# Kernel tuning notes

Hardware: AMD Instinct MI355X
Metric: run time of the kernel (lower is better)

## Reference

```python
import jax, jax.numpy as jnp
import numpy as np

N = 50000   # num_node
E = 1600000 # edge_size (N * avg_degree 32)
B = 64      # batch, hardcoded via repeat(64,1,1) in the torch module


def setup_inputs() -> dict:
    key = jax.random.key(0)
    k = jax.random.split(key, 8)
    return {
        "t": jax.random.normal(k[0], (1,), dtype=jnp.float32),
        "input": jax.random.normal(k[1], (B, N), dtype=jnp.float32),
        "edge_i": jax.random.randint(k[2], (E,), 0, N, dtype=jnp.int32),
        "edge_j": jax.random.randint(k[3], (E,), 0, N, dtype=jnp.int32),
        "weight_react": jax.random.normal(k[4], (1, E), dtype=jnp.float32) / 10.0,
        "weight_diff": jax.random.normal(k[5], (1, E), dtype=jnp.float32) / 1000.0,
        "bias_reaction": jax.random.normal(k[6], (1, N), dtype=jnp.float32) / 10.0,
        "bias_diffusion": jax.random.normal(k[7], (1, N), dtype=jnp.float32) / 10.0,
    }


def _lap_matvec(x, w, src, dst, n):
    # W[src_e, dst_e] = w_e (duplicates coalesce by sum, as torch sparse_coo_tensor does)
    # L = diag(colsum(W)) - W ; returns x @ L^T applied batched: out[b, v] = (L x[b])[v]
    col = jax.ops.segment_sum(w, dst, num_segments=n)                 # [N] column sums
    msg = jax.ops.segment_sum(w[:, None] * x[:, dst].T, src,
                              num_segments=n)                          # [N, B]
    return col[None, :] * x - msg.T                                   # [B, N]


def reference(t, input, edge_i, edge_j, weight_react, weight_diff,
              bias_reaction, bias_diffusion):
    x = input                                                          # [B, N]
    n = x.shape[1]
    # reaction Laplacian uses edges (i -> j); diffusion uses transposed (j -> i)
    reaction = _lap_matvec(x, weight_react[0], edge_i, edge_j, n) + bias_reaction
    diffusion = _lap_matvec(x, weight_diff[0], edge_j, edge_i, n) + bias_diffusion
    # up and down both True: tanh(reaction) + diffusion + input
    return jnp.tanh(reaction) + diffusion + x
```

## Files before the change

kernel.cpp:

```cpp
#include <hip/hip_runtime.h>
#include <hip/hip_fp16.h>


#define BKT_SHIFT 7
#define BKT_NODES 128
#define RCAP 4608
#define CH 4096
#define NBP 512

#define RFL(x) __builtin_amdgcn_readfirstlane(x)

__device__ __forceinline__ unsigned bf16_rne(float f) {
    unsigned u = __float_as_uint(f);
    unsigned rb = (u >> 16) & 1u;
    u += 0x7FFFu + rb;
    return u >> 16;
}
__device__ __forceinline__ float bf16_lo(int y) {
    return __uint_as_float(((unsigned)y) << 16);
}

__global__ void zero_kernel(float4* __restrict__ p, int n4) {
    int i = blockIdx.x * blockDim.x + threadIdx.x;
    int s = gridDim.x * blockDim.x;
    float4 z = make_float4(0.f, 0.f, 0.f, 0.f);
    for (; i < n4; i += s) p[i] = z;
}

__global__ void transpose_kernel(const float* __restrict__ x, float* __restrict__ xt,
                                 __half* __restrict__ xth, int N) {
    __shared__ float tile[64][65];
    int v0 = blockIdx.x * 64;
    int tx = threadIdx.x;
    int ty = threadIdx.y;
    if (v0 + tx < N) {
        for (int b = ty; b < 64; b += 16)
            tile[tx][b] = x[b * N + v0 + tx];
    }
    __syncthreads();
    for (int vl = ty; vl < 64; vl += 16) {
        int v = v0 + vl;
        if (v < N) {
            float val = tile[vl][tx];
            xt[(size_t)v * 64 + tx] = val;
            xth[(size_t)v * 64 + tx] = __float2half(val);
        }
    }
}

__global__ void __launch_bounds__(512) partition_kernel(
        const int* __restrict__ ei, const int* __restrict__ ej,
        const float* __restrict__ wr, const float* __restrict__ wd,
        int* __restrict__ gcur, int2* __restrict__ runs,
        int E, int NB) {
    __shared__ int cnt[2 * NBP];
    __shared__ int base_a[2 * NBP];
    __shared__ int gb[2 * NBP];
    __shared__ int2 buf[2 * CH];

    int tid = threadIdx.x;
    int e0 = blockIdx.x * CH;
    int ch_len = min(CH, E - e0);
    if (ch_len <= 0) return;

    for (int b = tid; b < 2 * NBP; b += 512) cnt[b] = 0;
    __syncthreads();
    for (int t = tid; t < ch_len; t += 512) {
        int i = ei[e0 + t], j = ej[e0 + t];
        atomicAdd(&cnt[i >> BKT_SHIFT], 1);
        atomicAdd(&cnt[NBP + (j >> BKT_SHIFT)], 1);
    }
    __syncthreads();
    if (tid < 64) {
        int carry = 0;
        #pragma unroll
        for (int c = 0; c < (2 * NBP) / 64; ++c) {
            int idx = c * 64 + tid;
            int val = cnt[idx];
            int scan = val;
            for (int off = 1; off < 64; off <<= 1) {
                int n = __shfl_up(scan, off, 64);
                if (tid >= off) scan += n;
            }
            int excl = scan - val + carry;
            base_a[idx] = excl;
            cnt[idx] = excl;
            carry += __shfl(scan, 63, 64);
        }
    }
    __syncthreads();
    for (int t = tid; t < ch_len; t += 512) {
        int e = e0 + t;
        int i = ei[e], j = ej[e];
        float wrv = wr[e], wdv = wd[e];
        unsigned br16 = bf16_rne(wrv), bd16 = bf16_rne(wdv);
        int b0 = i >> BKT_SHIFT;
        int p0 = atomicAdd(&cnt[b0], 1);
        buf[p0] = make_int2((int)(((unsigned)b0 << 23) | ((unsigned)(i & 127) << 16) | (unsigned)j),
                            (int)((br16 << 16) | bd16));
        int b1 = j >> BKT_SHIFT;
        int p1 = atomicAdd(&cnt[NBP + b1], 1);
        buf[p1] = make_int2((int)(((unsigned)b1 << 23) | ((unsigned)(j & 127) << 16) | (unsigned)i),
                            (int)((bd16 << 16) | br16));
    }
    __syncthreads();
    for (int cb = tid; cb < 2 * NBP; cb += 512) {
        int n = cnt[cb] - base_a[cb];
        if (n > 0) {
            int side = cb >> 9;
            int bkt = cb & (NBP - 1);
            gb[cb] = atomicAdd(&gcur[side * NB + bkt], n);
        }
    }
    __syncthreads();
    int total = 2 * ch_len;
    for (int t = tid; t < total; t += 512) {
        int2 p = buf[t];
        int side = (t >= ch_len) ? 1 : 0;
        int bkt = ((unsigned)p.x >> 23) & 0x1FF;
        int cb = side * NBP + bkt;
        int rank = gb[cb] + (t - base_a[cb]);
        if (rank < RCAP)
            runs[((size_t)(side * NB + bkt)) * RCAP + rank] = p;
    }
}

__global__ void __launch_bounds__(512) csr_kernel(
        const int* __restrict__ gcur, int2* __restrict__ runs,
        int4* __restrict__ meta, int NB, int N) {
    __shared__ int cnt[BKT_NODES];
    __shared__ int cur[BKT_NODES];
    __shared__ float csum[BKT_NODES];
    __shared__ int2 src[RCAP];
    __shared__ int2 dst[RCAP];

    int sb = blockIdx.x;
    int side = (sb >= NB) ? 1 : 0;
    int b = sb - side * NB;
    int v0 = b << BKT_SHIFT;
    int len = min(gcur[sb], RCAP);
    size_t roff = (size_t)sb * RCAP;
    int tid = threadIdx.x;

    if (tid < BKT_NODES) { cnt[tid] = 0; csum[tid] = 0.f; }
    __syncthreads();
    for (int k = tid; k < len; k += 512) {
        int2 p = runs[roff + k];
        src[k] = p;
        int dl = ((unsigned)p.x >> 16) & 0x7F;
        atomicAdd(&cnt[dl], 1);
        atomicAdd(&csum[dl], bf16_lo(p.y));
    }
    __syncthreads();
    if (tid < 64) {
        int carry = 0;
        #pragma unroll
        for (int c = 0; c < BKT_NODES / 64; ++c) {
            int idx = c * 64 + tid;
            int val = cnt[idx];
            int scan = val;
            for (int off = 1; off < 64; off <<= 1) {
                int n = __shfl_up(scan, off, 64);
                if (tid >= off) scan += n;
            }
            cur[idx] = scan - val + carry;
            carry += __shfl(scan, 63, 64);
        }
    }
    __syncthreads();
    if (tid < BKT_NODES) {
        int v = v0 + tid;
        if (v < N)
            meta[(size_t)side * N + v] =
                make_int4((int)roff + cur[tid], cnt[tid], __float_as_int(csum[tid]), 0);
    }
    __syncthreads();
    for (int k = tid; k < len; k += 512) {
        int2 p = src[k];
        int dl = ((unsigned)p.x >> 16) & 0x7F;
        int pos = atomicAdd(&cur[dl], 1);
        dst[pos] = p;
    }
    __syncthreads();
    for (int k = tid; k < len; k += 512)
        runs[roff + k] = dst[k];
}

__device__ __forceinline__ float seg_accum(const int2* __restrict__ seg, int n,
                                           const __half* __restrict__ xth, int lane) {
    float acc = 0.f;
    int k = 0;
    for (; k + 8 <= n; k += 8) {
        int2 p0 = seg[k + 0], p1 = seg[k + 1], p2 = seg[k + 2], p3 = seg[k + 3];
        int2 p4 = seg[k + 4], p5 = seg[k + 5], p6 = seg[k + 6], p7 = seg[k + 7];
        int o0 = RFL(p0.x) & 0xFFFF; int o1 = RFL(p1.x) & 0xFFFF;
        int o2 = RFL(p2.x) & 0xFFFF; int o3 = RFL(p3.x) & 0xFFFF;
        int o4 = RFL(p4.x) & 0xFFFF; int o5 = RFL(p5.x) & 0xFFFF;
        int o6 = RFL(p6.x) & 0xFFFF; int o7 = RFL(p7.x) & 0xFFFF;
        float x0 = __half2float(xth[((size_t)o0 << 6) + lane]);
        float x1 = __half2float(xth[((size_t)o1 << 6) + lane]);
        float x2 = __half2float(xth[((size_t)o2 << 6) + lane]);
        float x3 = __half2float(xth[((size_t)o3 << 6) + lane]);
        float x4 = __half2float(xth[((size_t)o4 << 6) + lane]);
        float x5 = __half2float(xth[((size_t)o5 << 6) + lane]);
        float x6 = __half2float(xth[((size_t)o6 << 6) + lane]);
        float x7 = __half2float(xth[((size_t)o7 << 6) + lane]);
        float w0 = __uint_as_float((unsigned)RFL(p0.y) & 0xFFFF0000u);
        float w1 = __uint_as_float((unsigned)RFL(p1.y) & 0xFFFF0000u);
        float w2 = __uint_as_float((unsigned)RFL(p2.y) & 0xFFFF0000u);
        float w3 = __uint_as_float((unsigned)RFL(p3.y) & 0xFFFF0000u);
        float w4 = __uint_as_float((unsigned)RFL(p4.y) & 0xFFFF0000u);
        float w5 = __uint_as_float((unsigned)RFL(p5.y) & 0xFFFF0000u);
        float w6 = __uint_as_float((unsigned)RFL(p6.y) & 0xFFFF0000u);
        float w7 = __uint_as_float((unsigned)RFL(p7.y) & 0xFFFF0000u);
        acc = fmaf(w0, x0, acc); acc = fmaf(w1, x1, acc);
        acc = fmaf(w2, x2, acc); acc = fmaf(w3, x3, acc);
        acc = fmaf(w4, x4, acc); acc = fmaf(w5, x5, acc);
        acc = fmaf(w6, x6, acc); acc = fmaf(w7, x7, acc);
    }
    for (; k < n; ++k) {
        int2 p = seg[k];
        int o = RFL(p.x) & 0xFFFF;
        float w = __uint_as_float((unsigned)RFL(p.y) & 0xFFFF0000u);
        acc = fmaf(w, __half2float(xth[((size_t)o << 6) + lane]), acc);
    }
    return acc;
}

__global__ void __launch_bounds__(256) gather_kernel(
        const float* __restrict__ xt, const __half* __restrict__ xth,
        const int4* __restrict__ meta, const int2* __restrict__ runs,
        const float* __restrict__ br, const float* __restrict__ bd,
        float* __restrict__ outt, int N) {
    int lane = threadIdx.x & 63;
    int v = RFL(blockIdx.x * 4 + (threadIdx.x >> 6));
    if (v >= N) return;
    int4 mr = meta[v];
    int4 md = meta[(size_t)N + v];
    int rbase = RFL(mr.x), rn = RFL(mr.y);
    int dbase = RFL(md.x), dn = RFL(md.y);
    float cold = __int_as_float(RFL(mr.z));
    float colr = __int_as_float(RFL(md.z));

    float accr = seg_accum(runs + rbase, rn, xth, lane);
    float accd = seg_accum(runs + dbase, dn, xth, lane);

    float xv = xt[((size_t)v << 6) + lane];
    float r = colr * xv - accr + br[v];
    float d = cold * xv - accd + bd[v];
    outt[((size_t)v << 6) + lane] = tanhf(r) + d + xv;
}

__global__ void transpose_out_kernel(const float* __restrict__ outt,
                                     float* __restrict__ out, int N) {
    __shared__ float tile[64][65];
    int v0 = blockIdx.x * 64;
    int tx = threadIdx.x;
    int ty = threadIdx.y;
    for (int vl = ty; vl < 64; vl += 16) {
        int v = v0 + vl;
        if (v < N)
            tile[vl][tx] = outt[(size_t)v * 64 + tx];
    }
    __syncthreads();
    if (v0 + tx < N) {
        for (int b = ty; b < 64; b += 16)
            out[b * N + v0 + tx] = tile[tx][b];
    }
}

extern "C" void kernel_launch(void* const* d_in, const int* in_sizes, int n_in,
                              void* d_out, int out_size, void* d_ws, size_t ws_size,
                              hipStream_t stream) {
    const float* x  = (const float*)d_in[1];
    const int*   ei = (const int*)d_in[2];
    const int*   ej = (const int*)d_in[3];
    const float* wr = (const float*)d_in[4];
    const float* wd = (const float*)d_in[5];
    const float* br = (const float*)d_in[6];
    const float* bd = (const float*)d_in[7];
    float* out = (float*)d_out;

    int E = in_sizes[2];
    int N = in_sizes[6];
    int NB = (N + BKT_NODES - 1) >> BKT_SHIFT;
    (void)out_size; (void)ws_size; (void)n_in;

    char* w = (char*)d_ws;
    float* xt   = (float*)w;   w += (size_t)N * 64 * 4;
    float* outt = (float*)w;   w += (size_t)N * 64 * 4;
    __half* xth = (__half*)w;  w += (size_t)N * 64 * 2;
    int* gcur   = (int*)w;     w += (size_t)((2 * NB + 3) / 4) * 4 * 4;
    w = (char*)(((uintptr_t)w + 15) & ~(uintptr_t)15);
    int4* meta  = (int4*)w;    w += (size_t)2 * N * 16;
    int2* runs  = (int2*)w;

    zero_kernel<<<4, 256, 0, stream>>>((float4*)gcur, (2 * NB + 3) / 4);

    dim3 tb(64, 16);
    int ntiles = (N + 63) / 64;
    transpose_kernel<<<ntiles, tb, 0, stream>>>(x, xt, xth, N);

    int nchunks = (E + CH - 1) / CH;
    partition_kernel<<<nchunks, 512, 0, stream>>>(ei, ej, wr, wd, gcur, runs, E, NB);

    csr_kernel<<<2 * NB, 512, 0, stream>>>(gcur, runs, meta, NB, N);

    int gblocks = (N + 3) / 4;
    gather_kernel<<<gblocks, 256, 0, stream>>>(xt, xth, meta, runs, br, bd, outt, N);

    transpose_out_kernel<<<ntiles, tb, 0, stream>>>(outt, out, N);
}
```

Baseline: 226.0 us.

## Compact CSR to 4-byte padded entries and gather two edges per wave with half2

The CSR kernel now packs each edge into one int (bf16 weight in the high half, source index in the low half) and pads every node's segment to a multiple of four. It writes the result to a separate runs2 buffer. The gather kernel reads segments as int4 and lets each half-wave handle a different edge, loading half2 values, then combines the halves with a cross-lane shuffle. The fp32 transposed copy of x is dropped, so the self term also comes from the fp16 copy. This cuts index traffic and load-instruction count in the gather, at the cost of lower precision in the self term and extra padding work.

```diff
diff --git a/kernel.cpp b/kernel.cpp
--- a/kernel.cpp
+++ b/kernel.cpp
@@ -5,6 +5,7 @@
 #define BKT_SHIFT 7
 #define BKT_NODES 128
 #define RCAP 4608
+#define RCAP2 4992
 #define CH 4096
 #define NBP 512
 
@@ -27,8 +28,7 @@
     for (; i < n4; i += s) p[i] = z;
 }
 
-__global__ void transpose_kernel(const float* __restrict__ x, float* __restrict__ xt,
-                                 __half* __restrict__ xth, int N) {
+__global__ void transpose_kernel(const float* __restrict__ x, __half* __restrict__ xth, int N) {
     __shared__ float tile[64][65];
     int v0 = blockIdx.x * 64;
     int tx = threadIdx.x;
@@ -40,11 +40,8 @@
     __syncthreads();
     for (int vl = ty; vl < 64; vl += 16) {
         int v = v0 + vl;
-        if (v < N) {
-            float val = tile[vl][tx];
-            xt[(size_t)v * 64 + tx] = val;
-            xth[(size_t)v * 64 + tx] = __float2half(val);
-        }
+        if (v < N)
+            xth[(size_t)v * 64 + tx] = __float2half(tile[vl][tx]);
     }
 }
 
@@ -126,13 +123,16 @@
 }
 
 __global__ void __launch_bounds__(512) csr_kernel(
-        const int* __restrict__ gcur, int2* __restrict__ runs,
-        int4* __restrict__ meta, int NB, int N) {
+        const int* __restrict__ gcur, const int2* __restrict__ runs,
+        int* __restrict__ runs2, int4* __restrict__ meta, int NB, int N) {
     __shared__ int cnt[BKT_NODES];
     __shared__ int cur[BKT_NODES];
+    __shared__ int pb[BKT_NODES];
     __shared__ float csum[BKT_NODES];
-    __shared__ int2 src[RCAP];
-    __shared__ int2 dst[RCAP];
+    __shared__ int src_c[RCAP];
+    __shared__ unsigned char dlb[RCAP];
+    __shared__ int dst[RCAP2];
+    __shared__ int total_s;
 
     int sb = blockIdx.x;
     int side = (sb >= NB) ? 1 : 0;
@@ -140,14 +140,16 @@
     int v0 = b << BKT_SHIFT;
     int len = min(gcur[sb], RCAP);
     size_t roff = (size_t)sb * RCAP;
+    size_t roff2 = (size_t)sb * RCAP2;
     int tid = threadIdx.x;
 
     if (tid < BKT_NODES) { cnt[tid] = 0; csum[tid] = 0.f; }
     __syncthreads();
     for (int k = tid; k < len; k += 512) {
         int2 p = runs[roff + k];
-        src[k] = p;
         int dl = ((unsigned)p.x >> 16) & 0x7F;
+        src_c[k] = (int)(((unsigned)p.y & 0xFFFF0000u) | ((unsigned)p.x & 0xFFFFu));
+        dlb[k] = (unsigned char)dl;
         atomicAdd(&cnt[dl], 1);
         atomicAdd(&csum[dl], bf16_lo(p.y));
     }
@@ -157,83 +159,63 @@
         #pragma unroll
         for (int c = 0; c < BKT_NODES / 64; ++c) {
             int idx = c * 64 + tid;
-            int val = cnt[idx];
+            int val = (cnt[idx] + 3) & ~3;
             int scan = val;
             for (int off = 1; off < 64; off <<= 1) {
                 int n = __shfl_up(scan, off, 64);
                 if (tid >= off) scan += n;
             }
-            cur[idx] = scan - val + carry;
+            int excl = scan - val + carry;
+            pb[idx] = excl;
+            cur[idx] = excl;
             carry += __shfl(scan, 63, 64);
         }
+        if (tid == 63) total_s = carry;
     }
     __syncthreads();
     if (tid < BKT_NODES) {
         int v = v0 + tid;
         if (v < N)
             meta[(size_t)side * N + v] =
-                make_int4((int)roff + cur[tid], cnt[tid], __float_as_int(csum[tid]), 0);
+                make_int4((int)(roff2 + pb[tid]), cnt[tid], __float_as_int(csum[tid]), 0);
+        int pc = (cnt[tid] + 3) & ~3;
+        for (int t = cnt[tid]; t < pc; ++t) dst[pb[tid] + t] = 0;
     }
     __syncthreads();
     for (int k = tid; k < len; k += 512) {
-        int2 p = src[k];
-        int dl = ((unsigned)p.x >> 16) & 0x7F;
+        int dl = dlb[k];
         int pos = atomicAdd(&cur[dl], 1);
-        dst[pos] = p;
-    }
-    __syncthreads();
-    for (int k = tid; k < len; k += 512)
-        runs[roff + k] = dst[k];
-}
-
-__device__ __forceinline__ float seg_accum(const int2* __restrict__ seg, int n,
-                                           const __half* __restrict__ xth, int lane) {
-    float acc = 0.f;
-    int k = 0;
-    for (; k + 8 <= n; k += 8) {
-        int2 p0 = seg[k + 0], p1 = seg[k + 1], p2 = seg[k + 2], p3 = seg[k + 3];
-        int2 p4 = seg[k + 4], p5 = seg[k + 5], p6 = seg[k + 6], p7 = seg[k + 7];
-        int o0 = RFL(p0.x) & 0xFFFF; int o1 = RFL(p1.x) & 0xFFFF;
-        int o2 = RFL(p2.x) & 0xFFFF; int o3 = RFL(p3.x) & 0xFFFF;
-        int o4 = RFL(p4.x) & 0xFFFF; int o5 = RFL(p5.x) & 0xFFFF;
-        int o6 = RFL(p6.x) & 0xFFFF; int o7 = RFL(p7.x) & 0xFFFF;
-        float x0 = __half2float(xth[((size_t)o0 << 6) + lane]);
-        float x1 = __half2float(xth[((size_t)o1 << 6) + lane]);
-        float x2 = __half2float(xth[((size_t)o2 << 6) + lane]);
-        float x3 = __half2float(xth[((size_t)o3 << 6) + lane]);
-        float x4 = __half2float(xth[((size_t)o4 << 6) + lane]);
-        float x5 = __half2float(xth[((size_t)o5 << 6) + lane]);
-        float x6 = __half2float(xth[((size_t)o6 << 6) + lane]);
-        float x7 = __half2float(xth[((size_t)o7 << 6) + lane]);
-        float w0 = __uint_as_float((unsigned)RFL(p0.y) & 0xFFFF0000u);
-        float w1 = __uint_as_float((unsigned)RFL(p1.y) & 0xFFFF0000u);
-        float w2 = __uint_as_float((unsigned)RFL(p2.y) & 0xFFFF0000u);
-        float w3 = __uint_as_float((unsigned)RFL(p3.y) & 0xFFFF0000u);
-        float w4 = __uint_as_float((unsigned)RFL(p4.y) & 0xFFFF0000u);
-        float w5 = __uint_as_float((unsigned)RFL(p5.y) & 0xFFFF0000u);
-        float w6 = __uint_as_float((unsigned)RFL(p6.y) & 0xFFFF0000u);
-        float w7 = __uint_as_float((unsigned)RFL(p7.y) & 0xFFFF0000u);
-        acc = fmaf(w0, x0, acc); acc = fmaf(w1, x1, acc);
-        acc = fmaf(w2, x2, acc); acc = fmaf(w3, x3, acc);
-        acc = fmaf(w4, x4, acc); acc = fmaf(w5, x5, acc);
-        acc = fmaf(w6, x6, acc); acc = fmaf(w7, x7, acc);
-    }
-    for (; k < n; ++k) {
-        int2 p = seg[k];
-        int o = RFL(p.x) & 0xFFFF;
-        float w = __uint_as_float((unsigned)RFL(p.y) & 0xFFFF0000u);
-        acc = fmaf(w, __half2float(xth[((size_t)o << 6) + lane]), acc);
-    }
-    return acc;
+        dst[pos] = src_c[k];
+    }
+    __syncthreads();
+    int total = total_s;
+    for (int k = tid; k < total; k += 512)
+        runs2[roff2 + k] = dst[k];
+}
+
+__device__ __forceinline__ void pair_acc(int pA, int pB,
+                                         const __half2* __restrict__ xth2,
+                                         int halfl, bool hi, float2& acc) {
+    int oA = RFL(pA) & 0xFFFF;
+    int oB = RFL(pB) & 0xFFFF;
+    float wA = __uint_as_float((unsigned)RFL(pA) & 0xFFFF0000u);
+    float wB = __uint_as_float((unsigned)RFL(pB) & 0xFFFF0000u);
+    int o = hi ? oB : oA;
+    float w = hi ? wB : wA;
+    float2 xf = __half22float2(xth2[((size_t)o << 5) + halfl]);
+    acc.x = fmaf(w, xf.x, acc.x);
+    acc.y = fmaf(w, xf.y, acc.y);
 }
 
 __global__ void __launch_bounds__(256) gather_kernel(
-        const float* __restrict__ xt, const __half* __restrict__ xth,
-        const int4* __restrict__ meta, const int2* __restrict__ runs,
+        const __half2* __restrict__ xth2, const int* __restrict__ runs2,
+        const int4* __restrict__ meta,
         const float* __restrict__ br, const float* __restrict__ bd,
-        float* __restrict__ outt, int N) {
+        float2* __restrict__ outt2, int N) {
     int lane = threadIdx.x & 63;
-    int v = RFL(blockIdx.x * 4 + (threadIdx.x >> 6));
+    int halfl = lane & 31;
+    bool hi = lane >= 32;
+    int v = blockIdx.x * 4 + (threadIdx.x >> 6);
     if (v >= N) return;
     int4 mr = meta[v];
     int4 md = meta[(size_t)N + v];
@@ -242,13 +224,41 @@
     float cold = __int_as_float(RFL(mr.z));
     float colr = __int_as_float(RFL(md.z));
 
-    float accr = seg_accum(runs + rbase, rn, xth, lane);
-    float accd = seg_accum(runs + dbase, dn, xth, lane);
-
-    float xv = xt[((size_t)v << 6) + lane];
-    float r = colr * xv - accr + br[v];
-    float d = cold * xv - accd + bd[v];
-    outt[((size_t)v << 6) + lane] = tanhf(r) + d + xv;
+    const int4* sr = (const int4*)(runs2 + rbase);
+    const int4* sd = (const int4*)(runs2 + dbase);
+    int nqr = (rn + 3) >> 2;
+    int nqd = (dn + 3) >> 2;
+    int nq = max(nqr, nqd);
+    float2 accr = make_float2(0.f, 0.f);
+    float2 accd = make_float2(0.f, 0.f);
+    for (int q = 0; q < nq; ++q) {
+        if (q < nqr) {
+            int4 qa = sr[q];
+            pair_acc(qa.x, qa.y, xth2, halfl, hi, accr);
+            pair_acc(qa.z, qa.w, xth2, halfl, hi, accr);
+        }
+        if (q < nqd) {
+            int4 qb = sd[q];
+            pair_acc(qb.x, qb.y, xth2, halfl, hi, accd);
+            pair_acc(qb.z, qb.w, xth2, halfl, hi, accd);
+        }
+    }
+    accr.x += __shfl_xor(accr.x, 32);
+    accr.y += __shfl_xor(accr.y, 32);
+    accd.x += __shfl_xor(accd.x, 32);
+    accd.y += __shfl_xor(accd.y, 32);
+
+    float brv = br[v], bdv = bd[v];
+    float2 xv = __half22float2(xth2[((size_t)v << 5) + halfl]);
+    float r0 = colr * xv.x - accr.x + brv;
+    float r1 = colr * xv.y - accr.y + brv;
+    float d0 = cold * xv.x - accd.x + bdv;
+    float d1 = cold * xv.y - accd.y + bdv;
+    float2 res;
+    res.x = tanhf(r0) + d0 + xv.x;
+    res.y = tanhf(r1) + d1 + xv.y;
+    if (!hi)
+        outt2[((size_t)v << 5) + halfl] = res;
 }
 
 __global__ void transpose_out_kernel(const float* __restrict__ outt,
@@ -287,27 +297,28 @@
     (void)out_size; (void)ws_size; (void)n_in;
 
     char* w = (char*)d_ws;
-    float* xt   = (float*)w;   w += (size_t)N * 64 * 4;
     float* outt = (float*)w;   w += (size_t)N * 64 * 4;
     __half* xth = (__half*)w;  w += (size_t)N * 64 * 2;
     int* gcur   = (int*)w;     w += (size_t)((2 * NB + 3) / 4) * 4 * 4;
     w = (char*)(((uintptr_t)w + 15) & ~(uintptr_t)15);
     int4* meta  = (int4*)w;    w += (size_t)2 * N * 16;
-    int2* runs  = (int2*)w;
+    int2* runs  = (int2*)w;    w += (size_t)2 * NB * RCAP * 8;
+    int* runs2  = (int*)w;
 
     zero_kernel<<<4, 256, 0, stream>>>((float4*)gcur, (2 * NB + 3) / 4);
 
     dim3 tb(64, 16);
     int ntiles = (N + 63) / 64;
-    transpose_kernel<<<ntiles, tb, 0, stream>>>(x, xt, xth, N);
+    transpose_kernel<<<ntiles, tb, 0, stream>>>(x, xth, N);
 
     int nchunks = (E + CH - 1) / CH;
     partition_kernel<<<nchunks, 512, 0, stream>>>(ei, ej, wr, wd, gcur, runs, E, NB);
 
-    csr_kernel<<<2 * NB, 512, 0, stream>>>(gcur, runs, meta, NB, N);
+    csr_kernel<<<2 * NB, 512, 0, stream>>>(gcur, runs, runs2, meta, NB, N);
 
     int gblocks = (N + 3) / 4;
-    gather_kernel<<<gblocks, 256, 0, stream>>>(xt, xth, meta, runs, br, bd, outt, N);
+    gather_kernel<<<gblocks, 256, 0, stream>>>((const __half2*)xth, runs2, meta,
+                                               br, bd, (float2*)outt, N);
 
     transpose_out_kernel<<<ntiles, tb, 0, stream>>>(outt, out, N);
 }
```

Result: no change. 224.3 us (-0.8%).
